# Performance work log

Measured on AMD Instinct MI355X. Metric: run time of the kernel, lower is better.

## Reference

```python
import jax, jax.numpy as jnp
import numpy as np
from jax import lax

B, E, V, T = 16384, 256, 128, 16
TAU = 1.0


def _gru(x, h, Wih, Whh, bih, bhh):
    # torch.nn.GRUCell math
    gi = x @ Wih.T + bih
    gh = h @ Whh.T + bhh
    ir, iz, i_n = jnp.split(gi, 3, axis=-1)
    hr, hz, h_n = jnp.split(gh, 3, axis=-1)
    r = jax.nn.sigmoid(ir + hr)
    z = jax.nn.sigmoid(iz + hz)
    n = jnp.tanh(i_n + r * h_n)
    return (1.0 - z) * n + z * h


def setup_inputs() -> dict:
    key = jax.random.key(0)
    ks = jax.random.split(key, 10)
    s = 0.05
    w = lambda k, shape: jax.random.normal(k, shape, jnp.float32) * s
    return {
        "x": jax.random.normal(ks[0], (B, E), jnp.float32),
        "global_idxes": jnp.arange(B, dtype=jnp.int32),
        "uniform_noise": jax.random.uniform(ks[1], (T, B, V), dtype=jnp.float32),
        "dec_Wd2e": w(ks[2], (E, V)), "dec_bd2e": jnp.zeros((E,), jnp.float32),
        "dec_Wih": w(ks[3], (3 * E, E)), "dec_Whh": w(ks[4], (3 * E, E)),
        "dec_bih": jnp.zeros((3 * E,), jnp.float32), "dec_bhh": jnp.zeros((3 * E,), jnp.float32),
        "dec_We2d": w(ks[5], (V, E)), "dec_be2d": jnp.zeros((V,), jnp.float32),
        "enc_Wd2e": w(ks[6], (E, V)), "enc_bd2e": jnp.zeros((E,), jnp.float32),
        "enc_Wih": w(ks[7], (3 * E, E)), "enc_Whh": w(ks[8], (3 * E, E)),
        "enc_bih": jnp.zeros((3 * E,), jnp.float32), "enc_bhh": jnp.zeros((3 * E,), jnp.float32),
    }


def _forward(x, uniform_noise,
             dec_Wd2e, dec_bd2e, dec_Wih, dec_Whh, dec_bih, dec_bhh, dec_We2d, dec_be2d,
             enc_Wd2e, enc_bd2e, enc_Wih, enc_Whh, enc_bih, enc_bhh):
    Bn = x.shape[0]
    # gumbel noise from pre-sampled uniforms (deterministic)
    gnoise = -jnp.log(-jnp.log(uniform_noise + 1e-10) + 1e-10)  # [T,B,V]

    # ---- GumbelDecoder: sequential GRUCell decode with alive/dead masking ----
    def dec_step(carry, g_t):
        state, last_tok, alive, N, t = carry
        emb = last_tok @ dec_Wd2e.T + dec_bd2e
        state = _gru(emb, state, dec_Wih, dec_Whh, dec_bih, dec_bhh)
        logits = state @ dec_We2d.T + dec_be2d
        y_soft = jax.nn.softmax((logits + g_t) / TAU, axis=-1)
        idx = jnp.argmax(y_soft, axis=-1)
        y_hard = jax.nn.one_hot(idx, V, dtype=y_soft.dtype)
        # straight-through hard gumbel-softmax
        y = y_soft + lax.stop_gradient(y_hard - y_soft)
        ended = idx == 0  # token 0 is the terminator
        N = jnp.where(ended, jnp.minimum(N, t), N)
        alive = alive & (~ended)
        # dead rows (incl. newly ended) have their token zeroed, as in torch
        y = jnp.where(alive[:, None], y, 0.0)
        return (state, y, alive, N, t + 1), y

    init = (x, jnp.zeros((Bn, V), x.dtype), jnp.ones((Bn,), bool),
            jnp.full((Bn,), T, jnp.int32), jnp.int32(0))
    (_, _, _, N, _), utt = lax.scan(dec_step, init, gnoise)  # utt: [T,B,V]

    # ---- OnehotEncoder: sequential GRUCell encode with alive sieve (masked) ----
    def enc_step(carry, u_t):
        state, out_state, alive = carry
        emb = u_t @ enc_Wd2e.T + enc_bd2e
        state = _gru(emb, state, enc_Wih, enc_Whh, enc_bih, enc_bhh)
        out_state = jnp.where(alive[:, None], state, out_state)
        ended = u_t[:, 0] > 0.5  # terminator seen in utterance
        alive = alive & (~ended)
        return (state, out_state, alive), None

    z0 = jnp.zeros((Bn, E), x.dtype)
    (_, reconst, _), _ = lax.scan(enc_step, (z0, z0, jnp.ones((Bn,), bool)), utt)

    utterance = jnp.transpose(utt, (1, 0, 2))  # [B,T,V]
    return utterance, N, reconst


def reference(x, global_idxes, uniform_noise,
              dec_Wd2e, dec_bd2e, dec_Wih, dec_Whh, dec_bih, dec_bhh, dec_We2d, dec_be2d,
              enc_Wd2e, enc_bd2e, enc_Wih, enc_Whh, enc_bih, enc_bhh):
    del global_idxes  # unused by the original forward
    return _forward(x, uniform_noise,
                    dec_Wd2e, dec_bd2e, dec_Wih, dec_Whh, dec_bih, dec_bhh, dec_We2d, dec_be2d,
                    enc_Wd2e, enc_bd2e, enc_Wih, enc_Whh, enc_bih, enc_bhh)
```

## Files before the change

kernel.cpp:

```cpp
#include <hip/hip_runtime.h>
#include <hip/hip_bf16.h>


namespace {
constexpr int kB  = 16384;
constexpr int kE  = 256;
constexpr int kV  = 128;
constexpr int kT  = 16;
constexpr int kG3 = 768;

constexpr int kOffWdhhT  = 0;
constexpr int kOffWehhT  = kG3 * kE;
constexpr int kOffWe2dT  = 2 * kG3 * kE;
constexpr int kOffDecTab = kOffWe2dT + kV * kE;
constexpr int kOffEncTab = kOffDecTab + 129 * kG3;
}

__device__ __forceinline__ float sigmf(float v) { return 1.0f / (1.0f + expf(-v)); }
__device__ __forceinline__ float gumbelf(float u) {
  return -logf(-logf(u + 1e-10f) + 1e-10f);
}

__global__ void prep_transpose(const float* __restrict__ dWhh,
                               const float* __restrict__ eWhh,
                               const float* __restrict__ We2d,
                               float* __restrict__ ws) {
  const int n1 = kG3 * kE;
  const int n2 = n1 + kG3 * kE;
  const int n3 = n2 + kV * kE;
  for (int i = blockIdx.x * blockDim.x + threadIdx.x; i < n3;
       i += gridDim.x * blockDim.x) {
    if (i < n1) {
      const int k = i / kG3, j = i - k * kG3;
      ws[i] = dWhh[j * kE + k];
    } else if (i < n2) {
      const int t = i - n1;
      const int k = t / kG3, j = t - k * kG3;
      ws[i] = eWhh[j * kE + k];
    } else {
      const int t = i - n2;
      const int k = t / kV, v = t - k * kV;
      ws[i] = We2d[v * kE + k];
    }
  }
}

__global__ void prep_tables(const float* __restrict__ Wih,
                            const float* __restrict__ Wd2e,
                            const float* __restrict__ bd2e,
                            const float* __restrict__ bih,
                            float* __restrict__ tab) {
  const int i = blockIdx.x * blockDim.x + threadIdx.x;
  if (i >= 129 * kG3) return;
  const int v = i / kG3, j = i - v * kG3;
  const float* wr = Wih + j * kE;
  float acc = 0.0f;
  if (v < kV) {
    for (int k = 0; k < kE; ++k) acc = fmaf(wr[k], Wd2e[k * kV + v] + bd2e[k], acc);
  } else {
    for (int k = 0; k < kE; ++k) acc = fmaf(wr[k], bd2e[k], acc);
  }
  tab[i] = acc + bih[j];
}

__device__ __forceinline__ void gru_half(float acc[8][3][4],
                                         const float (*__restrict__ h)[8],
                                         const float* __restrict__ WT,
                                         const int e0) {
#pragma unroll
  for (int r = 0; r < 8; ++r)
#pragma unroll
    for (int g = 0; g < 3; ++g)
#pragma unroll
      for (int c = 0; c < 4; ++c) acc[r][g][c] = 0.0f;
#pragma unroll 2
  for (int k = 0; k < kE; ++k) {
    const float4 hA = *(const float4*)(&h[k][0]);
    const float4 hB = *(const float4*)(&h[k][4]);
    const float* wp = WT + k * kG3 + e0;
    const float4 w0 = *(const float4*)(wp);
    const float4 w1 = *(const float4*)(wp + 256);
    const float4 w2 = *(const float4*)(wp + 512);
    const float hv[8] = {hA.x, hA.y, hA.z, hA.w, hB.x, hB.y, hB.z, hB.w};
    const float wv[3][4] = {{w0.x, w0.y, w0.z, w0.w},
                            {w1.x, w1.y, w1.z, w1.w},
                            {w2.x, w2.y, w2.z, w2.w}};
#pragma unroll
    for (int r = 0; r < 8; ++r)
#pragma unroll
      for (int g = 0; g < 3; ++g)
#pragma unroll
        for (int c = 0; c < 4; ++c)
          acc[r][g][c] = fmaf(hv[r], wv[g][c], acc[r][g][c]);
  }
}

__device__ __forceinline__ void gru_pointwise(float acc[8][3][4],
                                              float (*__restrict__ h)[8],
                                              const float* __restrict__ Tab,
                                              const int tok[8],
                                              const float4& br4, const float4& bz4,
                                              const float4& bn4, const int e0) {
  const float br[4] = {br4.x, br4.y, br4.z, br4.w};
  const float bz[4] = {bz4.x, bz4.y, bz4.z, bz4.w};
  const float bn[4] = {bn4.x, bn4.y, bn4.z, bn4.w};
#pragma unroll
  for (int r = 0; r < 8; ++r) {
    const float* gp = Tab + tok[r] * kG3 + e0;
    const float4 g0 = *(const float4*)(gp);
    const float4 g1 = *(const float4*)(gp + 256);
    const float4 g2 = *(const float4*)(gp + 512);
    const float gi[3][4] = {{g0.x, g0.y, g0.z, g0.w},
                            {g1.x, g1.y, g1.z, g1.w},
                            {g2.x, g2.y, g2.z, g2.w}};
#pragma unroll
    for (int c = 0; c < 4; ++c) {
      const float rg = sigmf(gi[0][c] + acc[r][0][c] + br[c]);
      const float zg = sigmf(gi[1][c] + acc[r][1][c] + bz[c]);
      const float ng = tanhf(gi[2][c] + rg * (acc[r][2][c] + bn[c]));
      acc[r][0][c] = ng;
      acc[r][1][c] = zg;
    }
  }
#pragma unroll
  for (int c = 0; c < 4; ++c) {
    const int e = e0 + c;
    const float4 hA = *(const float4*)(&h[e][0]);
    const float4 hB = *(const float4*)(&h[e][4]);
    const float ho[8] = {hA.x, hA.y, hA.z, hA.w, hB.x, hB.y, hB.z, hB.w};
    float hn[8];
#pragma unroll
    for (int r = 0; r < 8; ++r)
      hn[r] = (1.0f - acc[r][1][c]) * acc[r][0][c] + acc[r][1][c] * ho[r];
    *(float4*)(&h[e][0]) = make_float4(hn[0], hn[1], hn[2], hn[3]);
    *(float4*)(&h[e][4]) = make_float4(hn[4], hn[5], hn[6], hn[7]);
  }
}

__launch_bounds__(256, 2)
__global__ void gumbel_fused(const float* __restrict__ x,
                             const float* __restrict__ unoise,
                             const float* __restrict__ dbhh,
                             const float* __restrict__ dbe2d,
                             const float* __restrict__ ebhh,
                             const float* __restrict__ ws,
                             float* __restrict__ out) {
  const float* WdhhT  = ws + kOffWdhhT;
  const float* WehhT  = ws + kOffWehhT;
  const float* We2dT  = ws + kOffWe2dT;
  const float* DecTab = ws + kOffDecTab;
  const float* EncTab = ws + kOffEncTab;

  __shared__ float hbuf[2][4][kE][8];

  const int tid  = (int)threadIdx.x;
  const int w    = tid >> 6;
  const int jx   = tid & 63;
  const int row0 = (int)blockIdx.x * 32 + w * 8;
  const int e0   = jx * 4;

  float (*hd)[8] = hbuf[0][w];
  float (*he)[8] = hbuf[1][w];

  for (int i = jx; i < kE * 8; i += 64) {
    const int r = i >> 8, k = i & (kE - 1);
    hd[k][r] = x[(size_t)(row0 + r) * kE + k];
    he[k][r] = 0.0f;
  }
  __syncthreads();

  int tok[8], Nn[8];
  bool alive[8];
#pragma unroll
  for (int r = 0; r < 8; ++r) { tok[r] = kV; Nn[r] = kT; alive[r] = true; }

  const float4 dbr = *(const float4*)(dbhh + e0);
  const float4 dbz = *(const float4*)(dbhh + 256 + e0);
  const float4 dbn = *(const float4*)(dbhh + 512 + e0);
  const float4 ebr = *(const float4*)(ebhh + e0);
  const float4 ebz = *(const float4*)(ebhh + 256 + e0);
  const float4 ebn = *(const float4*)(ebhh + 512 + e0);
  const float2 be2 = *(const float2*)(dbe2d + 2 * jx);

  float acc[8][3][4];

  for (int t = 0; t < kT; ++t) {
    gru_half(acc, hd, WdhhT, e0);
    gru_pointwise(acc, hd, DecTab, tok, dbr, dbz, dbn, e0);
    __syncthreads();

    float l0[8], l1[8];
#pragma unroll
    for (int r = 0; r < 8; ++r) { l0[r] = 0.0f; l1[r] = 0.0f; }
#pragma unroll 2
    for (int k = 0; k < kE; ++k) {
      const float4 hA = *(const float4*)(&hd[k][0]);
      const float4 hB = *(const float4*)(&hd[k][4]);
      const float2 wv = *(const float2*)(We2dT + k * kV + 2 * jx);
      const float hv[8] = {hA.x, hA.y, hA.z, hA.w, hB.x, hB.y, hB.z, hB.w};
#pragma unroll
      for (int r = 0; r < 8; ++r) {
        l0[r] = fmaf(hv[r], wv.x, l0[r]);
        l1[r] = fmaf(hv[r], wv.y, l1[r]);
      }
    }
    const float* up = unoise + ((size_t)t * kB + row0) * kV + 2 * jx;
#pragma unroll
    for (int r = 0; r < 8; ++r) {
      const float2 u = *(const float2*)(up + (size_t)r * kV);
      const float a0 = l0[r] + be2.x + gumbelf(u.x);
      const float a1 = l1[r] + be2.y + gumbelf(u.y);
      float mv; int mi;
      if (a1 > a0) { mv = a1; mi = 2 * jx + 1; } else { mv = a0; mi = 2 * jx; }
#pragma unroll
      for (int off = 32; off >= 1; off >>= 1) {
        const float ov = __shfl_xor(mv, off, 64);
        const int   oi = __shfl_xor(mi, off, 64);
        if (ov > mv || (ov == mv && oi < mi)) { mv = ov; mi = oi; }
      }
      const bool ended = (mi == 0);
      if (ended) Nn[r] = (Nn[r] < t) ? Nn[r] : t;
      const bool anew = alive[r] && !ended;
      alive[r] = anew;
      tok[r] = anew ? mi : kV;
      float2 pr;
      pr.x = (anew && mi == 2 * jx) ? 1.0f : 0.0f;
      pr.y = (anew && mi == 2 * jx + 1) ? 1.0f : 0.0f;
      *reinterpret_cast<float2*>(
          out + ((size_t)(row0 + r) * kT + t) * kV + 2 * jx) = pr;
    }

    gru_half(acc, he, WehhT, e0);
    gru_pointwise(acc, he, EncTab, tok, ebr, ebz, ebn, e0);
    __syncthreads();
  }

  const size_t uttN = (size_t)kB * kT * kV;
#pragma unroll
  for (int r = 0; r < 8; ++r)
    if (jx == r) out[uttN + row0 + r] = (float)Nn[r];
  for (int i = jx; i < kE * 8; i += 64) {
    const int r = i >> 8, k = i & (kE - 1);
    out[uttN + kB + (size_t)(row0 + r) * kE + k] = he[k][r];
  }
}

extern "C" void kernel_launch(void* const* d_in, const int* in_sizes, int n_in,
                              void* d_out, int out_size, void* d_ws, size_t ws_size,
                              hipStream_t stream) {
  (void)in_sizes; (void)n_in; (void)out_size; (void)ws_size;
  const float* x      = (const float*)d_in[0];
  const float* unoise = (const float*)d_in[2];
  const float* dWd2e  = (const float*)d_in[3];
  const float* dbd2e  = (const float*)d_in[4];
  const float* dWih   = (const float*)d_in[5];
  const float* dWhh   = (const float*)d_in[6];
  const float* dbih   = (const float*)d_in[7];
  const float* dbhh   = (const float*)d_in[8];
  const float* dWe2d  = (const float*)d_in[9];
  const float* dbe2d  = (const float*)d_in[10];
  const float* eWd2e  = (const float*)d_in[11];
  const float* ebd2e  = (const float*)d_in[12];
  const float* eWih   = (const float*)d_in[13];
  const float* eWhh   = (const float*)d_in[14];
  const float* ebih   = (const float*)d_in[15];
  const float* ebhh   = (const float*)d_in[16];
  float* ws = (float*)d_ws;

  prep_transpose<<<1664, 256, 0, stream>>>(dWhh, eWhh, dWe2d, ws);
  prep_tables<<<(129 * kG3 + 255) / 256, 256, 0, stream>>>(
      dWih, dWd2e, dbd2e, dbih, ws + kOffDecTab);
  prep_tables<<<(129 * kG3 + 255) / 256, 256, 0, stream>>>(
      eWih, eWd2e, ebd2e, ebih, ws + kOffEncTab);
  gumbel_fused<<<kB / 32, 256, 0, stream>>>(
      x, unoise, dbhh, dbe2d, ebhh, ws, (float*)d_out);
}
```

Before: 3.442 ms.

## Share 16-row hidden state across block, one hidden unit per thread

```diff
diff --git a/kernel.cpp b/kernel.cpp
--- a/kernel.cpp
+++ b/kernel.cpp
@@ -1,5 +1,4 @@
 #include <hip/hip_runtime.h>
-#include <hip/hip_bf16.h>
 
 
 namespace {
@@ -8,6 +7,7 @@
 constexpr int kV  = 128;
 constexpr int kT  = 16;
 constexpr int kG3 = 768;
+constexpr int kR  = 16;
 
 constexpr int kOffWdhhT  = 0;
 constexpr int kOffWehhT  = kG3 * kE;
@@ -63,81 +63,58 @@
   tab[i] = acc + bih[j];
 }
 
-__device__ __forceinline__ void gru_half(float acc[8][3][4],
-                                         const float (*__restrict__ h)[8],
-                                         const float* __restrict__ WT,
-                                         const int e0) {
-#pragma unroll
-  for (int r = 0; r < 8; ++r)
-#pragma unroll
-    for (int g = 0; g < 3; ++g)
-#pragma unroll
-      for (int c = 0; c < 4; ++c) acc[r][g][c] = 0.0f;
+__device__ __forceinline__ void mv16(float acc[kR][3], const float (*h)[kR],
+                                     const float* __restrict__ WT, const int u) {
+#pragma unroll
+  for (int r = 0; r < kR; ++r) { acc[r][0] = 0.f; acc[r][1] = 0.f; acc[r][2] = 0.f; }
+  const float* wp = WT + u;
 #pragma unroll 2
   for (int k = 0; k < kE; ++k) {
     const float4 hA = *(const float4*)(&h[k][0]);
     const float4 hB = *(const float4*)(&h[k][4]);
-    const float* wp = WT + k * kG3 + e0;
-    const float4 w0 = *(const float4*)(wp);
-    const float4 w1 = *(const float4*)(wp + 256);
-    const float4 w2 = *(const float4*)(wp + 512);
-    const float hv[8] = {hA.x, hA.y, hA.z, hA.w, hB.x, hB.y, hB.z, hB.w};
-    const float wv[3][4] = {{w0.x, w0.y, w0.z, w0.w},
-                            {w1.x, w1.y, w1.z, w1.w},
-                            {w2.x, w2.y, w2.z, w2.w}};
-#pragma unroll
-    for (int r = 0; r < 8; ++r)
-#pragma unroll
-      for (int g = 0; g < 3; ++g)
-#pragma unroll
-        for (int c = 0; c < 4; ++c)
-          acc[r][g][c] = fmaf(hv[r], wv[g][c], acc[r][g][c]);
-  }
-}
-
-__device__ __forceinline__ void gru_pointwise(float acc[8][3][4],
-                                              float (*__restrict__ h)[8],
-                                              const float* __restrict__ Tab,
-                                              const int tok[8],
-                                              const float4& br4, const float4& bz4,
-                                              const float4& bn4, const int e0) {
-  const float br[4] = {br4.x, br4.y, br4.z, br4.w};
-  const float bz[4] = {bz4.x, bz4.y, bz4.z, bz4.w};
-  const float bn[4] = {bn4.x, bn4.y, bn4.z, bn4.w};
-#pragma unroll
-  for (int r = 0; r < 8; ++r) {
-    const float* gp = Tab + tok[r] * kG3 + e0;
-    const float4 g0 = *(const float4*)(gp);
-    const float4 g1 = *(const float4*)(gp + 256);
-    const float4 g2 = *(const float4*)(gp + 512);
-    const float gi[3][4] = {{g0.x, g0.y, g0.z, g0.w},
-                            {g1.x, g1.y, g1.z, g1.w},
-                            {g2.x, g2.y, g2.z, g2.w}};
-#pragma unroll
-    for (int c = 0; c < 4; ++c) {
-      const float rg = sigmf(gi[0][c] + acc[r][0][c] + br[c]);
-      const float zg = sigmf(gi[1][c] + acc[r][1][c] + bz[c]);
-      const float ng = tanhf(gi[2][c] + rg * (acc[r][2][c] + bn[c]));
-      acc[r][0][c] = ng;
-      acc[r][1][c] = zg;
+    const float4 hC = *(const float4*)(&h[k][8]);
+    const float4 hD = *(const float4*)(&h[k][12]);
+    const float w0 = wp[0], w1 = wp[kE], w2 = wp[2 * kE];
+    wp += kG3;
+    const float hv[kR] = {hA.x, hA.y, hA.z, hA.w, hB.x, hB.y, hB.z, hB.w,
+                          hC.x, hC.y, hC.z, hC.w, hD.x, hD.y, hD.z, hD.w};
+#pragma unroll
+    for (int r = 0; r < kR; ++r) {
+      acc[r][0] = fmaf(hv[r], w0, acc[r][0]);
+      acc[r][1] = fmaf(hv[r], w1, acc[r][1]);
+      acc[r][2] = fmaf(hv[r], w2, acc[r][2]);
     }
   }
-#pragma unroll
-  for (int c = 0; c < 4; ++c) {
-    const int e = e0 + c;
-    const float4 hA = *(const float4*)(&h[e][0]);
-    const float4 hB = *(const float4*)(&h[e][4]);
-    const float ho[8] = {hA.x, hA.y, hA.z, hA.w, hB.x, hB.y, hB.z, hB.w};
-    float hn[8];
-#pragma unroll
-    for (int r = 0; r < 8; ++r)
-      hn[r] = (1.0f - acc[r][1][c]) * acc[r][0][c] + acc[r][1][c] * ho[r];
-    *(float4*)(&h[e][0]) = make_float4(hn[0], hn[1], hn[2], hn[3]);
-    *(float4*)(&h[e][4]) = make_float4(hn[4], hn[5], hn[6], hn[7]);
-  }
-}
-
-__launch_bounds__(256, 2)
+}
+
+__device__ __forceinline__ void pw16(const float acc[kR][3], float (*h)[kR],
+                                     const float* __restrict__ Tab,
+                                     const int* toks,
+                                     const float br, const float bz,
+                                     const float bn, const int u) {
+  const float4 o0 = *(const float4*)(&h[u][0]);
+  const float4 o1 = *(const float4*)(&h[u][4]);
+  const float4 o2 = *(const float4*)(&h[u][8]);
+  const float4 o3 = *(const float4*)(&h[u][12]);
+  const float ho[kR] = {o0.x, o0.y, o0.z, o0.w, o1.x, o1.y, o1.z, o1.w,
+                        o2.x, o2.y, o2.z, o2.w, o3.x, o3.y, o3.z, o3.w};
+  float hn[kR];
+#pragma unroll
+  for (int r = 0; r < kR; ++r) {
+    const float* gp = Tab + toks[r] * kG3 + u;
+    const float gr = gp[0], gz = gp[kE], gn = gp[2 * kE];
+    const float rg = sigmf(gr + acc[r][0] + br);
+    const float zg = sigmf(gz + acc[r][1] + bz);
+    const float ng = tanhf(gn + rg * (acc[r][2] + bn));
+    hn[r] = (1.0f - zg) * ng + zg * ho[r];
+  }
+  *(float4*)(&h[u][0])  = make_float4(hn[0], hn[1], hn[2], hn[3]);
+  *(float4*)(&h[u][4])  = make_float4(hn[4], hn[5], hn[6], hn[7]);
+  *(float4*)(&h[u][8])  = make_float4(hn[8], hn[9], hn[10], hn[11]);
+  *(float4*)(&h[u][12]) = make_float4(hn[12], hn[13], hn[14], hn[15]);
+}
+
+__launch_bounds__(256, 4)
 __global__ void gumbel_fused(const float* __restrict__ x,
                              const float* __restrict__ unoise,
                              const float* __restrict__ dbhh,
@@ -151,95 +128,95 @@
   const float* DecTab = ws + kOffDecTab;
   const float* EncTab = ws + kOffEncTab;
 
-  __shared__ float hbuf[2][4][kE][8];
+  __shared__ float hd[kE][kR];
+  __shared__ float he[kE][kR];
+  __shared__ int   tok_sh[kR];
 
   const int tid  = (int)threadIdx.x;
   const int w    = tid >> 6;
   const int jx   = tid & 63;
-  const int row0 = (int)blockIdx.x * 32 + w * 8;
-  const int e0   = jx * 4;
-
-  float (*hd)[8] = hbuf[0][w];
-  float (*he)[8] = hbuf[1][w];
-
-  for (int i = jx; i < kE * 8; i += 64) {
+  const int row0 = (int)blockIdx.x * kR;
+  const int u    = tid;
+
+  for (int i = tid; i < kR * kE; i += 256) {
     const int r = i >> 8, k = i & (kE - 1);
     hd[k][r] = x[(size_t)(row0 + r) * kE + k];
     he[k][r] = 0.0f;
   }
+  if (tid < kR) tok_sh[tid] = kV;
   __syncthreads();
 
-  int tok[8], Nn[8];
-  bool alive[8];
-#pragma unroll
-  for (int r = 0; r < 8; ++r) { tok[r] = kV; Nn[r] = kT; alive[r] = true; }
-
-  const float4 dbr = *(const float4*)(dbhh + e0);
-  const float4 dbz = *(const float4*)(dbhh + 256 + e0);
-  const float4 dbn = *(const float4*)(dbhh + 512 + e0);
-  const float4 ebr = *(const float4*)(ebhh + e0);
-  const float4 ebz = *(const float4*)(ebhh + 256 + e0);
-  const float4 ebn = *(const float4*)(ebhh + 512 + e0);
+  float Nn[4];
+  bool alive[4];
+#pragma unroll
+  for (int q = 0; q < 4; ++q) { Nn[q] = (float)kT; alive[q] = true; }
+
+  const float dbr = dbhh[u], dbz = dbhh[kE + u], dbn = dbhh[2 * kE + u];
+  const float ebr = ebhh[u], ebz = ebhh[kE + u], ebn = ebhh[2 * kE + u];
   const float2 be2 = *(const float2*)(dbe2d + 2 * jx);
 
-  float acc[8][3][4];
+  float acc[kR][3];
 
   for (int t = 0; t < kT; ++t) {
-    gru_half(acc, hd, WdhhT, e0);
-    gru_pointwise(acc, hd, DecTab, tok, dbr, dbz, dbn, e0);
-    __syncthreads();
-
-    float l0[8], l1[8];
-#pragma unroll
-    for (int r = 0; r < 8; ++r) { l0[r] = 0.0f; l1[r] = 0.0f; }
+    mv16(acc, hd, WdhhT, u);
+    __syncthreads();
+    pw16(acc, hd, DecTab, tok_sh, dbr, dbz, dbn, u);
+    __syncthreads();
+
+    mv16(acc, he, WehhT, u);
+
+    {
+      float l0[4] = {0.f, 0.f, 0.f, 0.f}, l1[4] = {0.f, 0.f, 0.f, 0.f};
+      const float* wp2 = We2dT + 2 * jx;
 #pragma unroll 2
-    for (int k = 0; k < kE; ++k) {
-      const float4 hA = *(const float4*)(&hd[k][0]);
-      const float4 hB = *(const float4*)(&hd[k][4]);
-      const float2 wv = *(const float2*)(We2dT + k * kV + 2 * jx);
-      const float hv[8] = {hA.x, hA.y, hA.z, hA.w, hB.x, hB.y, hB.z, hB.w};
-#pragma unroll
-      for (int r = 0; r < 8; ++r) {
-        l0[r] = fmaf(hv[r], wv.x, l0[r]);
-        l1[r] = fmaf(hv[r], wv.y, l1[r]);
+      for (int k = 0; k < kE; ++k) {
+        const float2 wv = *(const float2*)wp2;
+        wp2 += kV;
+        const float4 hq = *(const float4*)(&hd[k][4 * w]);
+        const float hv[4] = {hq.x, hq.y, hq.z, hq.w};
+#pragma unroll
+        for (int q = 0; q < 4; ++q) {
+          l0[q] = fmaf(hv[q], wv.x, l0[q]);
+          l1[q] = fmaf(hv[q], wv.y, l1[q]);
+        }
+      }
+      const size_t rbase = (size_t)row0 + 4 * w;
+#pragma unroll
+      for (int q = 0; q < 4; ++q) {
+        const float2 uu =
+            *(const float2*)(unoise + ((size_t)t * kB + rbase + q) * kV + 2 * jx);
+        const float a0 = l0[q] + be2.x + gumbelf(uu.x);
+        const float a1 = l1[q] + be2.y + gumbelf(uu.y);
+        float mv; int mi;
+        if (a1 > a0) { mv = a1; mi = 2 * jx + 1; } else { mv = a0; mi = 2 * jx; }
+#pragma unroll
+        for (int off = 32; off >= 1; off >>= 1) {
+          const float ov = __shfl_xor(mv, off, 64);
+          const int   oi = __shfl_xor(mi, off, 64);
+          if (ov > mv || (ov == mv && oi < mi)) { mv = ov; mi = oi; }
+        }
+        const bool ended = (mi == 0);
+        if (ended) Nn[q] = fminf(Nn[q], (float)t);
+        const bool anew = alive[q] && !ended;
+        alive[q] = anew;
+        if (jx == 0) tok_sh[4 * w + q] = anew ? mi : kV;
+        float2 pr;
+        pr.x = (anew && mi == 2 * jx) ? 1.0f : 0.0f;
+        pr.y = (anew && mi == 2 * jx + 1) ? 1.0f : 0.0f;
+        *reinterpret_cast<float2*>(out + ((rbase + q) * kT + t) * kV + 2 * jx) = pr;
       }
     }
-    const float* up = unoise + ((size_t)t * kB + row0) * kV + 2 * jx;
-#pragma unroll
-    for (int r = 0; r < 8; ++r) {
-      const float2 u = *(const float2*)(up + (size_t)r * kV);
-      const float a0 = l0[r] + be2.x + gumbelf(u.x);
-      const float a1 = l1[r] + be2.y + gumbelf(u.y);
-      float mv; int mi;
-      if (a1 > a0) { mv = a1; mi = 2 * jx + 1; } else { mv = a0; mi = 2 * jx; }
-#pragma unroll
-      for (int off = 32; off >= 1; off >>= 1) {
-        const float ov = __shfl_xor(mv, off, 64);
-        const int   oi = __shfl_xor(mi, off, 64);
-        if (ov > mv || (ov == mv && oi < mi)) { mv = ov; mi = oi; }
-      }
-      const bool ended = (mi == 0);
-      if (ended) Nn[r] = (Nn[r] < t) ? Nn[r] : t;
-      const bool anew = alive[r] && !ended;
-      alive[r] = anew;
-      tok[r] = anew ? mi : kV;
-      float2 pr;
-      pr.x = (anew && mi == 2 * jx) ? 1.0f : 0.0f;
-      pr.y = (anew && mi == 2 * jx + 1) ? 1.0f : 0.0f;
-      *reinterpret_cast<float2*>(
-          out + ((size_t)(row0 + r) * kT + t) * kV + 2 * jx) = pr;
-    }
-
-    gru_half(acc, he, WehhT, e0);
-    gru_pointwise(acc, he, EncTab, tok, ebr, ebz, ebn, e0);
+    __syncthreads();
+    pw16(acc, he, EncTab, tok_sh, ebr, ebz, ebn, u);
     __syncthreads();
   }
 
   const size_t uttN = (size_t)kB * kT * kV;
-#pragma unroll
-  for (int r = 0; r < 8; ++r)
-    if (jx == r) out[uttN + row0 + r] = (float)Nn[r];
-  for (int i = jx; i < kE * 8; i += 64) {
+  if (jx == 0) {
+#pragma unroll
+    for (int q = 0; q < 4; ++q) out[uttN + row0 + 4 * w + q] = Nn[q];
+  }
+  for (int i = tid; i < kR * kE; i += 256) {
     const int r = i >> 8, k = i & (kE - 1);
     out[uttN + kB + (size_t)(row0 + r) * kE + k] = he[k][r];
   }
@@ -272,6 +249,6 @@
       dWih, dWd2e, dbd2e, dbih, ws + kOffDecTab);
   prep_tables<<<(129 * kG3 + 255) / 256, 256, 0, stream>>>(
       eWih, eWd2e, ebd2e, ebih, ws + kOffEncTab);
-  gumbel_fused<<<kB / 32, 256, 0, stream>>>(
+  gumbel_fused<<<kB / kR, 256, 0, stream>>>(
       x, unoise, dbhh, dbe2d, ebhh, ws, (float*)d_out);
 }
```

Measured after the change: 4.151 ms. 20.6% more time.
